# Optimization experiments

Hardware: AMD Instinct MI355X
Metric: run time of the kernel (lower is better)

Reference implementation:

```python
import jax, jax.numpy as jnp
import numpy as np

NUM_BLOCKS = 8
D = 1024          # residual_dim == attention_dim
FF = 4096         # feed_forward_dim
B, S = 4, 4096
EPS_ATTN = 1e-6
EPS_LN = 1e-6


def _ln(x, scale, bias):
    m = jnp.mean(x, axis=-1, keepdims=True)
    v = jnp.var(x, axis=-1, keepdims=True)
    return (x - m) * jax.lax.rsqrt(v + EPS_LN) * scale + bias


def setup_inputs() -> dict:
    key = jax.random.key(0)
    ks = jax.random.split(key, 16)
    g = lambda k, shape, fan: jax.random.normal(k, shape, jnp.float32) * (1.0 / np.sqrt(fan))
    inp = {
        "x": jax.random.normal(ks[0], (B, S, D), jnp.float32),
        "Wq": g(ks[1], (NUM_BLOCKS, D, D), D), "bq": jnp.zeros((NUM_BLOCKS, D), jnp.float32),
        "Wk": g(ks[2], (NUM_BLOCKS, D, D), D), "bk": jnp.zeros((NUM_BLOCKS, D), jnp.float32),
        "Wv": g(ks[3], (NUM_BLOCKS, D, D), D), "bv": jnp.zeros((NUM_BLOCKS, D), jnp.float32),
        "Wo": g(ks[4], (NUM_BLOCKS, D, D), D), "bo": jnp.zeros((NUM_BLOCKS, D), jnp.float32),
        "ln1_s": jnp.ones((NUM_BLOCKS, D), jnp.float32), "ln1_b": jnp.zeros((NUM_BLOCKS, D), jnp.float32),
        "W1": g(ks[5], (NUM_BLOCKS, D, FF), D), "b1": jnp.zeros((NUM_BLOCKS, FF), jnp.float32),
        "W2": g(ks[6], (NUM_BLOCKS, FF, D), FF), "b2": jnp.zeros((NUM_BLOCKS, D), jnp.float32),
        "ln2_s": jnp.ones((NUM_BLOCKS, D), jnp.float32), "ln2_b": jnp.zeros((NUM_BLOCKS, D), jnp.float32),
    }
    return inp


def _forward(x, Wq, bq, Wk, bk, Wv, bv, Wo, bo, ln1_s, ln1_b, W1, b1, W2, b2, ln2_s, ln2_b):
    gelu = lambda t: jax.nn.gelu(t, approximate=True)  # flax nn.gelu default
    fmap = lambda t: jax.nn.elu(t) + 1.0
    for i in range(NUM_BLOCKS):
        # --- linear attention sublayer ---
        residual = x
        Q = fmap(x @ Wq[i] + bq[i])          # [b, s, h]
        K = fmap(x @ Wk[i] + bk[i])          # [b, s, h]
        value = x @ Wv[i] + bv[i]            # [b, s, h]
        KV = jnp.einsum('nsh,nsh->nh', K, value)          # per-channel sum_s K*V
        Ksum = jnp.sum(K, axis=1)                         # [b, h]
        Z = 1.0 / (Q * Ksum[:, None, :] + EPS_ATTN)       # [b, s, h]
        V = Q * KV[:, None, :] * Z                        # [b, s, h]
        attn_out = gelu(V @ Wo[i] + bo[i])
        x = _ln(attn_out + residual, ln1_s[i], ln1_b[i])
        # --- feed-forward sublayer ---
        residual = x
        h = gelu(x @ W1[i] + b1[i])
        ff_out = gelu(h @ W2[i] + b2[i])
        x = _ln(ff_out + residual, ln2_s[i], ln2_b[i])
    return x


def reference(x, Wq, bq, Wk, bk, Wv, bv, Wo, bo, ln1_s, ln1_b, W1, b1, W2, b2, ln2_s, ln2_b):
    return _forward(x, Wq, bq, Wk, bk, Wv, bv, Wo, bo, ln1_s, ln1_b, W1, b1, W2, b2, ln2_s, ln2_b)
```

## Files before the change

### kernel.cpp

```cpp
#include <hip/hip_runtime.h>
#include <hip/hip_bf16.h>
#include <cstdint>

typedef unsigned short ushort_t;
typedef __attribute__((ext_vector_type(8))) short short8;
typedef __attribute__((ext_vector_type(4))) float floatx4;
typedef __attribute__((ext_vector_type(4))) ushort_t ushort4v;

#define DEVI __device__ __forceinline__

DEVI float b2f(ushort_t u){ union{unsigned int i; float f;} v; v.i = ((unsigned int)u)<<16; return v.f; }
DEVI ushort_t f2b(float f){ union{float f; unsigned int i;} v; v.f=f; unsigned int r = (v.i + 0x7FFFu + ((v.i>>16)&1u)) >> 16; return (ushort_t)r; }

DEVI float gelu_f(float t){
  float t3 = t*t*t;
  return 0.5f*t*(1.0f + tanhf(0.7978845608028654f*(t + 0.044715f*t3)));
}

#define GLD_LDS16(src, dst) \
  __builtin_amdgcn_global_load_lds((const __attribute__((address_space(1))) void*)(src), \
                                   (__attribute__((address_space(3))) void*)(dst), 16, 0, 0)

#define BAR()    asm volatile("s_barrier" ::: "memory")
#define WAITV(n) asm volatile("s_waitcnt vmcnt(" #n ")" ::: "memory")

#define MFMA16(d, a, b) d = __builtin_amdgcn_mfma_f32_16x16x32_bf16(a, b, d, 0, 0, 0)

template<int BUFOFF>
DEVI void ktile(const ushort_t* aB0, const ushort_t* aB1,
                const ushort_t* bB0, const ushort_t* bB1, floatx4 (&acc)[8][4])
{
  short8 af0[8], af1[8], bf0[4], bf1[4];
  #pragma unroll
  for (int mi = 0; mi < 8; mi++) af0[mi] = *(const short8*)(aB0 + BUFOFF + mi*1024);
  #pragma unroll
  for (int ni = 0; ni < 4; ni++) bf0[ni] = *(const short8*)(bB0 + BUFOFF + ni*1024);
  BAR();
  __builtin_amdgcn_s_setprio(1);
  #pragma unroll
  for (int mi = 0; mi < 8; mi++){ MFMA16(acc[mi][0], af0[mi], bf0[0]); MFMA16(acc[mi][1], af0[mi], bf0[1]); }
  __builtin_amdgcn_s_setprio(0);
  BAR();
  #pragma unroll
  for (int mi = 0; mi < 8; mi++) af1[mi] = *(const short8*)(aB1 + BUFOFF + mi*1024);
  bf1[0] = *(const short8*)(bB1 + BUFOFF);
  bf1[1] = *(const short8*)(bB1 + BUFOFF + 1024);
  BAR();
  __builtin_amdgcn_s_setprio(1);
  #pragma unroll
  for (int mi = 0; mi < 8; mi++){ MFMA16(acc[mi][2], af0[mi], bf0[2]); MFMA16(acc[mi][3], af0[mi], bf0[3]); }
  __builtin_amdgcn_s_setprio(0);
  BAR();
  bf1[2] = *(const short8*)(bB1 + BUFOFF + 2048);
  bf1[3] = *(const short8*)(bB1 + BUFOFF + 3072);
  BAR();
  __builtin_amdgcn_s_setprio(1);
  #pragma unroll
  for (int mi = 0; mi < 8; mi++){ MFMA16(acc[mi][0], af1[mi], bf1[0]); MFMA16(acc[mi][1], af1[mi], bf1[1]); }
  __builtin_amdgcn_s_setprio(0);
  BAR();
  __builtin_amdgcn_s_setprio(1);
  #pragma unroll
  for (int mi = 0; mi < 8; mi++){ MFMA16(acc[mi][2], af1[mi], bf1[2]); MFMA16(acc[mi][3], af1[mi], bf1[3]); }
  __builtin_amdgcn_s_setprio(0);
  BAR();
}

DEVI void gemm_core(const ushort_t* __restrict__ A, const ushort_t* __restrict__ Bt,
                    int K, int tileM, int tileN, floatx4 (&acc)[8][4])
{
  __shared__ alignas(16) ushort_t As[2][16384];
  __shared__ alignas(16) ushort_t Bs[2][16384];
  const int tid  = threadIdx.x;
  const int wave = tid >> 6, lane = tid & 63;
  const int quad = lane >> 4, l16 = lane & 15;
  const int wm = wave >> 2, wn = wave & 3;

  const int rr = tid >> 3;
  const int gg = (tid & 7) ^ (rr & 7);
  const ushort_t* srcA = A  + (size_t)(tileM + rr) * K + gg * 8;
  const ushort_t* srcB = Bt + (size_t)(tileN + rr) * K + gg * 8;
  const size_t K64 = (size_t)K * 64;
  ushort_t* dstA = &As[0][0] + wave * 512;
  ushort_t* dstB = &Bs[0][0] + wave * 512;

#define STAGE2(sp, dp) do{ GLD_LDS16((sp), (dp)); GLD_LDS16((sp) + K64, (dp) + 4096); }while(0)

  const int s0 = (quad ^ (l16 & 7)) * 8;
  const int s1 = s0 ^ 32;
  const ushort_t* aB0 = &As[0][0] + (wm*128 + l16)*64 + s0;
  const ushort_t* aB1 = &As[0][0] + (wm*128 + l16)*64 + s1;
  const ushort_t* bB0 = &Bs[0][0] + (wn*64  + l16)*64 + s0;
  const ushort_t* bB1 = &Bs[0][0] + (wn*64  + l16)*64 + s1;

  const int nkt = K >> 6;

  STAGE2(srcA,              dstA);
  STAGE2(srcA + 2*K64,      dstA + 8192);
  STAGE2(srcB,              dstB);
  STAGE2(srcB + 2*K64,      dstB + 8192);
  if (nkt > 1){
    STAGE2(srcA + 64,          dstA + 16384);
    STAGE2(srcA + 64 + 2*K64,  dstA + 16384 + 8192);
    STAGE2(srcB + 64,          dstB + 16384);
    WAITV(6);
  } else {
    WAITV(0);
  }
  BAR();

  for (int tt = 0; tt < nkt; tt += 2){
    STAGE2(srcB + (size_t)(tt+1)*64 + 2*K64, dstB + 16384 + 8192);
    ktile<0>(aB0, aB1, bB0, bB1, acc);
    if (tt + 2 < nkt){
      const size_t k8 = (size_t)(tt+2) * 64;
      STAGE2(srcA + k8,          dstA);
      STAGE2(srcA + k8 + 2*K64,  dstA + 8192);
      STAGE2(srcB + k8,          dstB);
      WAITV(6); BAR();
      STAGE2(srcB + k8 + 2*K64,  dstB + 8192);
    } else {
      WAITV(0); BAR();
    }
    ktile<16384>(aB0, aB1, bB0, bB1, acc);
    if (tt + 3 < nkt){
      const size_t k8 = (size_t)(tt+3) * 64;
      STAGE2(srcA + k8,          dstA + 16384);
      STAGE2(srcA + k8 + 2*K64,  dstA + 16384 + 8192);
      STAGE2(srcB + k8,          dstB + 16384);
      WAITV(6); BAR();
    }
  }
#undef STAGE2
}

template<int EPI>
__global__ __launch_bounds__(512, 2)
void gemm_kernel(const ushort_t* __restrict__ A, const ushort_t* __restrict__ Bt,
                 const float* __restrict__ bias, const float* __restrict__ res,
                 ushort_t* __restrict__ out, int N, int K)
{
  const int tileM = blockIdx.x * 256, tileN = blockIdx.y * 256;
  floatx4 acc[8][4] = {};
  gemm_core(A, Bt, K, tileM, tileN, acc);

  const int tid = threadIdx.x, wave = tid >> 6, lane = tid & 63;
  const int quad = lane >> 4, l16 = lane & 15;
  const int wm = wave >> 2, wn = wave & 3;

  float bv4[4];
  #pragma unroll
  for (int ni = 0; ni < 4; ni++) bv4[ni] = bias[tileN + wn * 64 + ni * 16 + l16];

  #pragma unroll
  for (int mi = 0; mi < 8; mi++){
    #pragma unroll
    for (int r = 0; r < 4; r++){
      const int row = tileM + wm * 128 + mi * 16 + quad * 4 + r;
      #pragma unroll
      for (int ni = 0; ni < 4; ni++){
        const int col = tileN + wn * 64 + ni * 16 + l16;
        float v = acc[mi][ni][r] + bv4[ni];
        if constexpr (EPI == 0){ v = (v > 0.f) ? (v + 1.f) : expf(v); }
        else if constexpr (EPI == 2){ v = gelu_f(v); }
        else if constexpr (EPI == 3){ v = gelu_f(v) + res[(size_t)row * N + col]; }
        out[(size_t)row * N + col] = f2b(v);
      }
    }
  }
}

__global__ __launch_bounds__(512, 2)
void qkv_gemm_kernel(const ushort_t* __restrict__ A, const ushort_t* __restrict__ Bt,
                     const float* __restrict__ bq, const float* __restrict__ bk,
                     const float* __restrict__ bv,
                     ushort_t* __restrict__ outQ, ushort_t* __restrict__ outK,
                     ushort_t* __restrict__ outV, int K)
{
  const int tileM = blockIdx.x * 256, tileN = blockIdx.y * 256;
  floatx4 acc[8][4] = {};
  gemm_core(A, Bt, K, tileM, tileN, acc);

  const int tid = threadIdx.x, wave = tid >> 6, lane = tid & 63;
  const int quad = lane >> 4, l16 = lane & 15;
  const int wm = wave >> 2, wn = wave & 3;

  const int seg  = tileN >> 10;
  const int nloc = tileN & 1023;
  const float* bias = (seg == 0) ? bq : (seg == 1) ? bk : bv;
  ushort_t* out     = (seg == 0) ? outQ : (seg == 1) ? outK : outV;

  float bv4[4];
  #pragma unroll
  for (int ni = 0; ni < 4; ni++) bv4[ni] = bias[nloc + wn * 64 + ni * 16 + l16];

  #pragma unroll
  for (int mi = 0; mi < 8; mi++){
    #pragma unroll
    for (int r = 0; r < 4; r++){
      const int row = tileM + wm * 128 + mi * 16 + quad * 4 + r;
      #pragma unroll
      for (int ni = 0; ni < 4; ni++){
        const int col = nloc + wn * 64 + ni * 16 + l16;
        float v = acc[mi][ni][r] + bv4[ni];
        if (seg < 2){ v = (v > 0.f) ? (v + 1.f) : expf(v); }
        out[(size_t)row * 1024 + col] = f2b(v);
      }
    }
  }
}

__global__ __launch_bounds__(256)
void reduce_kv_kernel(const ushort_t* __restrict__ Kb, const ushort_t* __restrict__ Vb,
                      float* __restrict__ KV, float* __restrict__ Ksum)
{
  const int b = blockIdx.x >> 6, chunk = blockIdx.x & 63;
  const int t = threadIdx.x;
  const size_t base = ((size_t)b*4096 + (size_t)chunk*64)*1024 + t*4;
  float kv[4] = {0,0,0,0}, ks[4] = {0,0,0,0};
  for (int s = 0; s < 64; s++){
    ushort4v kk = *(const ushort4v*)(Kb + base + (size_t)s*1024);
    ushort4v vv = *(const ushort4v*)(Vb + base + (size_t)s*1024);
    #pragma unroll
    for (int j = 0; j < 4; j++){ float kf = b2f(kk[j]); kv[j] += kf*b2f(vv[j]); ks[j] += kf; }
  }
  #pragma unroll
  for (int j = 0; j < 4; j++){
    atomicAdd(&KV[b*1024 + t*4 + j], kv[j]);
    atomicAdd(&Ksum[b*1024 + t*4 + j], ks[j]);
  }
}

__global__ __launch_bounds__(256)
void attn_map_kernel(ushort_t* __restrict__ Q, const float* __restrict__ KV, const float* __restrict__ Ksum)
{
  const size_t g = (size_t)blockIdx.x*256 + threadIdx.x;
  const size_t base = g*4;
  const int b  = (int)(base >> 22);
  const int h0 = (int)(base & 1023);
  ushort4v q4 = *(const ushort4v*)(Q + base);
  ushort4v o4;
  #pragma unroll
  for (int j = 0; j < 4; j++){
    float q = b2f(q4[j]);
    float v = q*KV[b*1024 + h0 + j] / (q*Ksum[b*1024 + h0 + j] + 1e-6f);
    o4[j] = f2b(v);
  }
  *(ushort4v*)(Q + base) = o4;
}

__global__ __launch_bounds__(256)
void ln_kernel(const ushort_t* __restrict__ y, const float* __restrict__ sc,
               const float* __restrict__ bi, ushort_t* __restrict__ xb, float* __restrict__ xf)
{
  const int row = blockIdx.x, t = threadIdx.x;
  const ushort_t* yr = y + (size_t)row*1024;
  ushort4v v4 = *(const ushort4v*)(yr + t*4);
  float f[4]; float s1 = 0.f, s2 = 0.f;
  #pragma unroll
  for (int j = 0; j < 4; j++){ f[j] = b2f(v4[j]); s1 += f[j]; s2 += f[j]*f[j]; }
  #pragma unroll
  for (int off = 32; off; off >>= 1){ s1 += __shfl_down(s1, off); s2 += __shfl_down(s2, off); }
  __shared__ float red[2][4];
  const int wave = t >> 6, lane = t & 63;
  if (lane == 0){ red[0][wave] = s1; red[1][wave] = s2; }
  __syncthreads();
  s1 = red[0][0] + red[0][1] + red[0][2] + red[0][3];
  s2 = red[1][0] + red[1][1] + red[1][2] + red[1][3];
  const float mean = s1 * (1.0f/1024.0f);
  const float var  = s2 * (1.0f/1024.0f) - mean*mean;
  const float inv  = rsqrtf(var + 1e-6f);
  ushort4v o4;
  #pragma unroll
  for (int j = 0; j < 4; j++){
    const int h = t*4 + j;
    const float o = (f[j] - mean)*inv*sc[h] + bi[h];
    o4[j] = f2b(o);
    xf[(size_t)row*1024 + h] = o;
  }
  *(ushort4v*)(xb + (size_t)row*1024 + t*4) = o4;
}

struct TParams { const float* src[6]; ushort_t* dst[6]; };

__global__ __launch_bounds__(256)
void transpose_all_kernel(TParams p)
{
  __shared__ float tile[32][33];
  const int id = blockIdx.x;
  int m, bx, by, R, C;
  if (id < 4096){ m = 4; int l = id;        bx = l & 127; by = l >> 7; R = 1024; C = 4096; }
  else if (id < 8192){ m = 5; int l = id - 4096; bx = l & 31; by = l >> 5; R = 4096; C = 1024; }
  else { int l = id - 8192; m = l >> 10; l &= 1023; bx = l & 31; by = l >> 5; R = 1024; C = 1024; }
  const float* in = p.src[m];
  ushort_t* out = p.dst[m];
  const int t = threadIdx.x;
  const int tx = t & 31, ty = t >> 5;
  const int rb = by*32, cb = bx*32;
  #pragma unroll
  for (int j = 0; j < 32; j += 8) tile[ty+j][tx] = in[(size_t)(rb+ty+j)*C + cb+tx];
  __syncthreads();
  #pragma unroll
  for (int j = 0; j < 32; j += 8) out[(size_t)(cb+ty+j)*R + rb+tx] = f2b(tile[tx][ty+j]);
}

__global__ __launch_bounds__(256)
void cvt_kernel(const float* __restrict__ in, ushort_t* __restrict__ out)
{
  const size_t base = ((size_t)blockIdx.x*256 + threadIdx.x)*4;
  ushort4v o4;
  #pragma unroll
  for (int j = 0; j < 4; j++) o4[j] = f2b(in[base + j]);
  *(ushort4v*)(out + base) = o4;
}

extern "C" void kernel_launch(void* const* d_in, const int* in_sizes, int n_in,
                              void* d_out, int out_size, void* d_ws, size_t ws_size,
                              hipStream_t stream)
{
  const float* x_in = (const float*)d_in[0];
  const float* Wq   = (const float*)d_in[1];
  const float* bq   = (const float*)d_in[2];
  const float* Wk   = (const float*)d_in[3];
  const float* bk   = (const float*)d_in[4];
  const float* Wv   = (const float*)d_in[5];
  const float* bv   = (const float*)d_in[6];
  const float* Wo   = (const float*)d_in[7];
  const float* bo   = (const float*)d_in[8];
  const float* ln1s = (const float*)d_in[9];
  const float* ln1b = (const float*)d_in[10];
  const float* W1   = (const float*)d_in[11];
  const float* b1   = (const float*)d_in[12];
  const float* W2   = (const float*)d_in[13];
  const float* b2   = (const float*)d_in[14];
  const float* ln2s = (const float*)d_in[15];
  const float* ln2b = (const float*)d_in[16];

  float* xf = (float*)d_out;

  char* ws = (char*)d_ws;
  const size_t MB = 1024*1024;
  ushort_t* xb     = (ushort_t*)(ws);
  char*     regB   = ws + 32*MB;
  ushort_t* bufQ   = (ushort_t*)(regB);
  ushort_t* bufK   = (ushort_t*)(regB + 32*MB);
  ushort_t* bufVal = (ushort_t*)(regB + 64*MB);
  ushort_t* bufH   = (ushort_t*)(regB);
  ushort_t* bufY   = (ushort_t*)(regB + 128*MB);
  ushort_t* WqkvT  = (ushort_t*)(ws + 192*MB);
  ushort_t* WoT    = (ushort_t*)(ws + 198*MB);
  ushort_t* W1T    = (ushort_t*)(ws + 200*MB);
  ushort_t* W2T    = (ushort_t*)(ws + 208*MB);
  float*    KV     = (float*)(ws + 216*MB);
  float*    Ksum   = (float*)(ws + 216*MB + 16*1024);

  const int M = 16384, D = 1024, FF = 4096;
  const dim3 blk(256);
  const dim3 blkG(512);

  hipMemcpyAsync(xf, x_in, (size_t)M*D*sizeof(float), hipMemcpyDeviceToDevice, stream);
  cvt_kernel<<<dim3(M*D/1024), blk, 0, stream>>>(x_in, xb);

  for (int i = 0; i < 8; i++){
    TParams tp;
    tp.src[0] = Wq + (size_t)i*D*D;  tp.dst[0] = WqkvT;
    tp.src[1] = Wk + (size_t)i*D*D;  tp.dst[1] = WqkvT + 1024*1024;
    tp.src[2] = Wv + (size_t)i*D*D;  tp.dst[2] = WqkvT + 2*1024*1024;
    tp.src[3] = Wo + (size_t)i*D*D;  tp.dst[3] = WoT;
    tp.src[4] = W1 + (size_t)i*D*FF; tp.dst[4] = W1T;
    tp.src[5] = W2 + (size_t)i*FF*D; tp.dst[5] = W2T;
    transpose_all_kernel<<<dim3(12288), blk, 0, stream>>>(tp);

    qkv_gemm_kernel<<<dim3(64, 12), blkG, 0, stream>>>(xb, WqkvT, bq + i*D, bk + i*D, bv + i*D,
                                                       bufQ, bufK, bufVal, D);

    hipMemsetAsync(KV, 0, 32*1024, stream);
    reduce_kv_kernel<<<dim3(256), blk, 0, stream>>>(bufK, bufVal, KV, Ksum);
    attn_map_kernel<<<dim3(16384), blk, 0, stream>>>(bufQ, KV, Ksum);

    gemm_kernel<3><<<dim3(64, 4), blkG, 0, stream>>>(bufQ, WoT, bo + i*D, xf, bufVal, D, D);
    ln_kernel<<<dim3(16384), blk, 0, stream>>>(bufVal, ln1s + i*D, ln1b + i*D, xb, xf);

    gemm_kernel<2><<<dim3(64, 16), blkG, 0, stream>>>(xb, W1T, b1 + i*FF, nullptr, bufH, FF, D);
    gemm_kernel<3><<<dim3(64, 4),  blkG, 0, stream>>>(bufH, W2T, b2 + i*D, xf, bufY, D, FF);
    ln_kernel<<<dim3(16384), blk, 0, stream>>>(bufY, ln2s + i*D, ln2b + i*D, xb, xf);
  }
  (void)in_sizes; (void)n_in; (void)out_size; (void)ws_size;
}
```

Before: 6.594 ms.

## Simplify GEMM k-loop to whole-tile double buffering without interleaved barriers

```diff
diff --git a/kernel.cpp b/kernel.cpp
--- a/kernel.cpp
+++ b/kernel.cpp
@@ -27,43 +27,26 @@
 #define MFMA16(d, a, b) d = __builtin_amdgcn_mfma_f32_16x16x32_bf16(a, b, d, 0, 0, 0)
 
 template<int BUFOFF>
-DEVI void ktile(const ushort_t* aB0, const ushort_t* aB1,
-                const ushort_t* bB0, const ushort_t* bB1, floatx4 (&acc)[8][4])
-{
-  short8 af0[8], af1[8], bf0[4], bf1[4];
-  #pragma unroll
-  for (int mi = 0; mi < 8; mi++) af0[mi] = *(const short8*)(aB0 + BUFOFF + mi*1024);
-  #pragma unroll
-  for (int ni = 0; ni < 4; ni++) bf0[ni] = *(const short8*)(bB0 + BUFOFF + ni*1024);
-  BAR();
-  __builtin_amdgcn_s_setprio(1);
-  #pragma unroll
-  for (int mi = 0; mi < 8; mi++){ MFMA16(acc[mi][0], af0[mi], bf0[0]); MFMA16(acc[mi][1], af0[mi], bf0[1]); }
-  __builtin_amdgcn_s_setprio(0);
-  BAR();
-  #pragma unroll
-  for (int mi = 0; mi < 8; mi++) af1[mi] = *(const short8*)(aB1 + BUFOFF + mi*1024);
-  bf1[0] = *(const short8*)(bB1 + BUFOFF);
-  bf1[1] = *(const short8*)(bB1 + BUFOFF + 1024);
-  BAR();
-  __builtin_amdgcn_s_setprio(1);
-  #pragma unroll
-  for (int mi = 0; mi < 8; mi++){ MFMA16(acc[mi][2], af0[mi], bf0[2]); MFMA16(acc[mi][3], af0[mi], bf0[3]); }
-  __builtin_amdgcn_s_setprio(0);
-  BAR();
-  bf1[2] = *(const short8*)(bB1 + BUFOFF + 2048);
-  bf1[3] = *(const short8*)(bB1 + BUFOFF + 3072);
-  BAR();
-  __builtin_amdgcn_s_setprio(1);
-  #pragma unroll
-  for (int mi = 0; mi < 8; mi++){ MFMA16(acc[mi][0], af1[mi], bf1[0]); MFMA16(acc[mi][1], af1[mi], bf1[1]); }
-  __builtin_amdgcn_s_setprio(0);
-  BAR();
-  __builtin_amdgcn_s_setprio(1);
-  #pragma unroll
-  for (int mi = 0; mi < 8; mi++){ MFMA16(acc[mi][2], af1[mi], bf1[2]); MFMA16(acc[mi][3], af1[mi], bf1[3]); }
-  __builtin_amdgcn_s_setprio(0);
-  BAR();
+DEVI void ktile2(const ushort_t* aB0, const ushort_t* aB1,
+                 const ushort_t* bB0, const ushort_t* bB1, floatx4 (&acc)[8][4])
+{
+  short8 a0[8], a1[8], b0[4], b1[4];
+  #pragma unroll
+  for (int mi = 0; mi < 8; mi++) a0[mi] = *(const short8*)(aB0 + BUFOFF + mi*1024);
+  #pragma unroll
+  for (int ni = 0; ni < 4; ni++) b0[ni] = *(const short8*)(bB0 + BUFOFF + ni*1024);
+  #pragma unroll
+  for (int mi = 0; mi < 8; mi++) a1[mi] = *(const short8*)(aB1 + BUFOFF + mi*1024);
+  #pragma unroll
+  for (int ni = 0; ni < 4; ni++) b1[ni] = *(const short8*)(bB1 + BUFOFF + ni*1024);
+  #pragma unroll
+  for (int ni = 0; ni < 4; ni++)
+    #pragma unroll
+    for (int mi = 0; mi < 8; mi++) MFMA16(acc[mi][ni], a0[mi], b0[ni]);
+  #pragma unroll
+  for (int ni = 0; ni < 4; ni++)
+    #pragma unroll
+    for (int mi = 0; mi < 8; mi++) MFMA16(acc[mi][ni], a1[mi], b1[ni]);
 }
 
 DEVI void gemm_core(const ushort_t* __restrict__ A, const ushort_t* __restrict__ Bt,
@@ -84,7 +67,17 @@
   ushort_t* dstA = &As[0][0] + wave * 512;
   ushort_t* dstB = &Bs[0][0] + wave * 512;
 
-#define STAGE2(sp, dp) do{ GLD_LDS16((sp), (dp)); GLD_LDS16((sp) + K64, (dp) + 4096); }while(0)
+#define STAGE_TILE(t, BO) do{ \
+    const size_t ko = (size_t)(t) * 64; \
+    GLD_LDS16(srcA + ko,          dstA + (BO)); \
+    GLD_LDS16(srcA + ko + K64,    dstA + (BO) + 4096); \
+    GLD_LDS16(srcA + ko + 2*K64,  dstA + (BO) + 8192); \
+    GLD_LDS16(srcA + ko + 3*K64,  dstA + (BO) + 12288); \
+    GLD_LDS16(srcB + ko,          dstB + (BO)); \
+    GLD_LDS16(srcB + ko + K64,    dstB + (BO) + 4096); \
+    GLD_LDS16(srcB + ko + 2*K64,  dstB + (BO) + 8192); \
+    GLD_LDS16(srcB + ko + 3*K64,  dstB + (BO) + 12288); \
+  }while(0)
 
   const int s0 = (quad ^ (l16 & 7)) * 8;
   const int s1 = s0 ^ 32;
@@ -95,43 +88,27 @@
 
   const int nkt = K >> 6;
 
-  STAGE2(srcA,              dstA);
-  STAGE2(srcA + 2*K64,      dstA + 8192);
-  STAGE2(srcB,              dstB);
-  STAGE2(srcB + 2*K64,      dstB + 8192);
-  if (nkt > 1){
-    STAGE2(srcA + 64,          dstA + 16384);
-    STAGE2(srcA + 64 + 2*K64,  dstA + 16384 + 8192);
-    STAGE2(srcB + 64,          dstB + 16384);
-    WAITV(6);
-  } else {
-    WAITV(0);
-  }
+  STAGE_TILE(0, 0);
+  STAGE_TILE(1, 16384);
+  WAITV(8);
   BAR();
 
   for (int tt = 0; tt < nkt; tt += 2){
-    STAGE2(srcB + (size_t)(tt+1)*64 + 2*K64, dstB + 16384 + 8192);
-    ktile<0>(aB0, aB1, bB0, bB1, acc);
-    if (tt + 2 < nkt){
-      const size_t k8 = (size_t)(tt+2) * 64;
-      STAGE2(srcA + k8,          dstA);
-      STAGE2(srcA + k8 + 2*K64,  dstA + 8192);
-      STAGE2(srcB + k8,          dstB);
-      WAITV(6); BAR();
-      STAGE2(srcB + k8 + 2*K64,  dstB + 8192);
-    } else {
-      WAITV(0); BAR();
+    ktile2<0>(aB0, aB1, bB0, bB1, acc);
+    BAR();
+    if (tt + 2 < nkt){ STAGE_TILE(tt + 2, 0); WAITV(8); }
+    else             { WAITV(0); }
+    BAR();
+    ktile2<16384>(aB0, aB1, bB0, bB1, acc);
+    if (tt + 3 < nkt){
+      BAR();
+      STAGE_TILE(tt + 3, 16384); WAITV(8);
+      BAR();
+    } else if (tt + 2 < nkt){
+      BAR(); WAITV(0); BAR();
     }
-    ktile<16384>(aB0, aB1, bB0, bB1, acc);
-    if (tt + 3 < nkt){
-      const size_t k8 = (size_t)(tt+3) * 64;
-      STAGE2(srcA + k8,          dstA + 16384);
-      STAGE2(srcA + k8 + 2*K64,  dstA + 16384 + 8192);
-      STAGE2(srcB + k8,          dstB + 16384);
-      WAITV(6); BAR();
-    }
-  }
-#undef STAGE2
+  }
+#undef STAGE_TILE
 }
 
 template<int EPI>
```

Measured after the change: 5.432 ms. 17.6% less time.
